# Kernel tuning notes

Measured on AMD Instinct MI355X. Metric: run time of the kernel, lower is better.

Reference implementation:

```python
import jax, jax.numpy as jnp
import numpy as np

N, E, CIN, COUT, T = 50000, 800000, 64, 64, 12


def setup_inputs() -> dict:
    key = jax.random.key(0)
    k1, k2, k3, k4, k5, k6 = jax.random.split(key, 6)
    x = jax.random.normal(k1, (N, CIN, T), dtype=jnp.float32)
    src = jax.random.randint(k2, (E,), 0, N, dtype=jnp.int32)
    dst = jax.random.randint(k3, (E,), 0, N, dtype=jnp.int32)
    edge_index = jnp.stack([src, dst], axis=0)
    edge_attr = jax.random.uniform(k4, (E,), dtype=jnp.float32)
    W = jax.random.normal(k5, (CIN, COUT), dtype=jnp.float32) / np.sqrt(CIN)
    b = jax.random.normal(k6, (COUT,), dtype=jnp.float32) * 0.01
    return {"x": x, "edge_index": edge_index, "edge_attr": edge_attr, "W": W, "b": b}


def reference(x, edge_index, edge_attr, W, b):
    # GCNConv applied independently to each of T temporal slices, then ReLU.
    n = x.shape[0]
    src, dst = edge_index[0], edge_index[1]
    # add self-loops with weight 1.0 (PyG GCNConv default)
    loop = jnp.arange(n, dtype=src.dtype)
    src_f = jnp.concatenate([src, loop])
    dst_f = jnp.concatenate([dst, loop])
    ew = jnp.concatenate([edge_attr, jnp.ones((n,), x.dtype)])
    # symmetric normalization: deg computed at target (col) nodes
    deg = jax.ops.segment_sum(ew, dst_f, num_segments=n)
    dis = jnp.where(deg > 0, jax.lax.rsqrt(deg), 0.0)
    norm = dis[src_f] * ew * dis[dst_f]  # (E+N,)

    def step(carry, x_t):  # x_t: (N, Cin)
        xw = x_t @ W                              # (N, Cout)
        msgs = xw[src_f] * norm[:, None]          # (E+N, Cout) gather
        out = jax.ops.segment_sum(msgs, dst_f, num_segments=n) + b
        return carry, jax.nn.relu(out)

    _, ys = jax.lax.scan(step, None, jnp.transpose(x, (2, 0, 1)))  # (T, N, Cout)
    return jnp.transpose(ys, (1, 2, 0))  # (N, Cout, T)
```

## Files before the change

### kernel.cpp

```cpp
#include <hip/hip_runtime.h>

#define CIN   64
#define COUT  64
#define TT    12
#define FEAT  (CIN * TT)
#define QROW  (FEAT / 4)

typedef unsigned int uint32;
typedef unsigned long long u64;

#define DEG_SCALE 1048576.0f

__global__ __launch_bounds__(256) void k_cvt(const float4* __restrict__ x,
                                             uint2* __restrict__ xh, int nquads) {
    int i = blockIdx.x * blockDim.x + threadIdx.x;
    int stride = gridDim.x * blockDim.x;
    for (; i < nquads; i += stride) {
        float4 v = x[i];
        uint32 u0 = __float_as_uint(v.x), u1 = __float_as_uint(v.y);
        uint32 u2 = __float_as_uint(v.z), u3 = __float_as_uint(v.w);
        u0 = (u0 + 0x7fffu + ((u0 >> 16) & 1)) >> 16;
        u1 = (u1 + 0x7fffu + ((u1 >> 16) & 1)) >> 16;
        u2 = (u2 + 0x7fffu + ((u2 >> 16) & 1)) >> 16;
        u3 = (u3 + 0x7fffu + ((u3 >> 16) & 1)) >> 16;
        uint2 o; o.x = u0 | (u1 << 16); o.y = u2 | (u3 << 16);
        xh[i] = o;
    }
}

__global__ void k_deg(const int* __restrict__ dst, const float* __restrict__ ea,
                      u64* __restrict__ deg64, int e_cnt) {
    int e = blockIdx.x * blockDim.x + threadIdx.x;
    if (e < e_cnt) {
        u64 v = ((u64)1 << 32) | (u64)(uint32)(ea[e] * DEG_SCALE + 0.5f);
        atomicAdd(&deg64[dst[e]], v);
    }
}

__global__ __launch_bounds__(256) void k_disred(const u64* __restrict__ deg64,
                                                float* __restrict__ dis,
                                                int* __restrict__ partial, int n) {
    __shared__ int red[256];
    int t = threadIdx.x;
    int i = blockIdx.x * 256 + t;
    int cnt = 0;
    if (i < n) {
        u64 v = deg64[i];
        cnt = (int)(v >> 32);
        float deg = 1.0f + (float)(uint32)v * (1.0f / DEG_SCALE);
        dis[i] = rsqrtf(deg);
    }
    red[t] = cnt;
    __syncthreads();
    for (int off = 128; off > 0; off >>= 1) {
        if (t < off) red[t] += red[t + off];
        __syncthreads();
    }
    if (t == 0) partial[blockIdx.x] = red[0];
}

__global__ __launch_bounds__(1024) void k_scanpart(int* __restrict__ partial, int nb,
                                                   int* __restrict__ rowptrN) {
    __shared__ int tmp[1024];
    int t = threadIdx.x;
    int v = (t < nb) ? partial[t] : 0;
    tmp[t] = v;
    __syncthreads();
    for (int off = 1; off < 1024; off <<= 1) {
        int u = (t >= off) ? tmp[t - off] : 0;
        __syncthreads();
        tmp[t] += u;
        __syncthreads();
    }
    if (t < nb) partial[t] = tmp[t] - v;
    if (t == 1023) *rowptrN = tmp[1023];
}

__global__ __launch_bounds__(256) void k_scanwrite(const u64* __restrict__ deg64,
                                                   const int* __restrict__ partial,
                                                   int* __restrict__ rowptr,
                                                   int* __restrict__ cursor, int n) {
    __shared__ int tmp[256];
    int t = threadIdx.x;
    int i = blockIdx.x * 256 + t;
    int v = (i < n) ? (int)(deg64[i] >> 32) : 0;
    tmp[t] = v;
    __syncthreads();
    for (int off = 1; off < 256; off <<= 1) {
        int u = (t >= off) ? tmp[t - off] : 0;
        __syncthreads();
        tmp[t] += u;
        __syncthreads();
    }
    int excl = tmp[t] - v + partial[blockIdx.x];
    if (i < n) { rowptr[i] = excl; cursor[i] = excl; }
}

__global__ void k_fill(const int* __restrict__ src, const int* __restrict__ dst,
                       const float* __restrict__ ea, const float* __restrict__ dis,
                       int* __restrict__ cursor, int2* __restrict__ csr, int e_cnt) {
    int e = blockIdx.x * blockDim.x + threadIdx.x;
    if (e < e_cnt) {
        int s = src[e], d = dst[e];
        int pos = atomicAdd(&cursor[d], 1);
        float w = dis[s] * ea[e] * dis[d];
        int2 p; p.x = s; p.y = __float_as_int(w);
        csr[pos] = p;
    }
}

template <int BF16>
__global__ __launch_bounds__(192) void k_conv(
    const void* __restrict__ xsrc, const float* __restrict__ W,
    const float* __restrict__ b, const float* __restrict__ dis,
    const int* __restrict__ rowptr, const int2* __restrict__ csr,
    float* __restrict__ out)
{
    __shared__ float sAgg[FEAT];
    __shared__ float sB[COUT];

    const int n = blockIdx.x;
    const int t = threadIdx.x;
    if (t < COUT) sB[t] = b[t];

    const int start = rowptr[n];
    const int end   = rowptr[n + 1];
    const float dn  = dis[n];
    const float selfw = dn * dn;

    float a0, a1, a2, a3;
    if (BF16) {
        const uint2* xb = (const uint2*)xsrc;
        uint2 v = xb[(size_t)n * QROW + t];
        a0 = selfw * __uint_as_float(v.x << 16);
        a1 = selfw * __uint_as_float(v.x & 0xffff0000u);
        a2 = selfw * __uint_as_float(v.y << 16);
        a3 = selfw * __uint_as_float(v.y & 0xffff0000u);
    } else {
        const float4* xb = (const float4*)xsrc;
        float4 v = xb[(size_t)n * QROW + t];
        a0 = selfw * v.x; a1 = selfw * v.y; a2 = selfw * v.z; a3 = selfw * v.w;
    }

    for (int e = start; e < end; ++e) {
        int2 p = csr[e];
        int s   = p.x;
        float w = __int_as_float(p.y);
        if (BF16) {
            const uint2* xb = (const uint2*)xsrc;
            uint2 v = xb[(size_t)s * QROW + t];
            a0 = fmaf(w, __uint_as_float(v.x << 16),         a0);
            a1 = fmaf(w, __uint_as_float(v.x & 0xffff0000u), a1);
            a2 = fmaf(w, __uint_as_float(v.y << 16),         a2);
            a3 = fmaf(w, __uint_as_float(v.y & 0xffff0000u), a3);
        } else {
            const float4* xb = (const float4*)xsrc;
            float4 v = xb[(size_t)s * QROW + t];
            a0 = fmaf(w, v.x, a0); a1 = fmaf(w, v.y, a1);
            a2 = fmaf(w, v.z, a2); a3 = fmaf(w, v.w, a3);
        }
    }

    float4 av; av.x = a0; av.y = a1; av.z = a2; av.w = a3;
    *((float4*)&sAgg[4 * t]) = av;
    __syncthreads();

    const int co  = t & 63;
    const int tg  = t >> 6;
    const int tt0 = tg * 4;
    float o0 = sB[co], o1 = o0, o2 = o0, o3 = o0;
#pragma unroll
    for (int c = 0; c < CIN; ++c) {
        float wv = W[c * COUT + co];
        o0 = fmaf(wv, sAgg[c * TT + tt0    ], o0);
        o1 = fmaf(wv, sAgg[c * TT + tt0 + 1], o1);
        o2 = fmaf(wv, sAgg[c * TT + tt0 + 2], o2);
        o3 = fmaf(wv, sAgg[c * TT + tt0 + 3], o3);
    }
    o0 = fmaxf(o0, 0.0f); o1 = fmaxf(o1, 0.0f);
    o2 = fmaxf(o2, 0.0f); o3 = fmaxf(o3, 0.0f);

    __syncthreads();
    float4 ov; ov.x = o0; ov.y = o1; ov.z = o2; ov.w = o3;
    *((float4*)&sAgg[co * TT + tt0]) = ov;
    __syncthreads();
    *((float4*)(out + (size_t)n * FEAT + 4 * t)) = *((const float4*)&sAgg[4 * t]);
}

extern "C" void kernel_launch(void* const* d_in, const int* in_sizes, int n_in,
                              void* d_out, int out_size, void* d_ws, size_t ws_size,
                              hipStream_t stream) {
    const float* x   = (const float*)d_in[0];
    const int*   ei  = (const int*)d_in[1];
    const float* ea  = (const float*)d_in[2];
    const float* W   = (const float*)d_in[3];
    const float* b   = (const float*)d_in[4];
    float* out = (float*)d_out;

    const int E = in_sizes[2];
    const int N = in_sizes[0] / FEAT;
    const int* src = ei;
    const int* dst = ei + E;

    size_t off = 0;
    char* ws = (char*)d_ws;
    auto alloc = [&](size_t bytes) -> char* {
        char* p = ws + off;
        off = (off + bytes + 15) & ~(size_t)15;
        return p;
    };
    u64*   deg64   = (u64*)  alloc((size_t)N * 8);
    float* dis     = (float*)alloc((size_t)N * 4);
    int*   rowptr  = (int*)  alloc((size_t)(N + 1) * 4);
    int*   cursor  = (int*)  alloc((size_t)N * 4);
    int*   partial = (int*)  alloc(4096);
    int2*  csr     = (int2*) alloc((size_t)E * 8);
    unsigned short* xh = (unsigned short*)alloc((size_t)N * FEAT * 2);
    const bool use_bf16 = (off <= ws_size);

    int nb_e = (E + 255) / 256;
    int nb_n = (N + 255) / 256;

    hipMemsetAsync(deg64, 0, (size_t)N * 8, stream);
    if (use_bf16) {
        int nquads = (N * FEAT) / 4;
        k_cvt<<<2048, 256, 0, stream>>>((const float4*)x, (uint2*)xh, nquads);
    }
    k_deg      <<<nb_e, 256, 0, stream>>>(dst, ea, deg64, E);
    k_disred   <<<nb_n, 256, 0, stream>>>(deg64, dis, partial, N);
    k_scanpart <<<1, 1024, 0, stream>>>(partial, nb_n, rowptr + N);
    k_scanwrite<<<nb_n, 256, 0, stream>>>(deg64, partial, rowptr, cursor, N);
    k_fill     <<<nb_e, 256, 0, stream>>>(src, dst, ea, dis, cursor, csr, E);
    if (use_bf16)
        k_conv<1><<<N, 192, 0, stream>>>(xh, W, b, dis, rowptr, csr, out);
    else
        k_conv<0><<<N, 192, 0, stream>>>(x,  W, b, dis, rowptr, csr, out);
}
```

Measured before the change: 355.1 us.

## Fuse convert with degree count, merge scan kernels, stage edges in LDS

Merges the bf16 conversion and degree atomics into one launch with block-range dispatch, and folds the single-block partial scan into the per-block scan by having each block reduce its predecessors' partials. The conv kernel now stages CSR entries cooperatively in shared memory in chunks of 192, and uses nontemporal loads and stores for the streaming input and output. The aim is fewer launches and less per-thread redundant CSR loading. The cost is extra barriers in the edge loop, and a scan that assumes at most 256 partial blocks.

```diff
diff --git a/kernel.cpp b/kernel.cpp
--- a/kernel.cpp
+++ b/kernel.cpp
@@ -8,32 +8,36 @@
 
 typedef unsigned int uint32;
 typedef unsigned long long u64;
+typedef float  __attribute__((ext_vector_type(4))) f32x4;
 
 #define DEG_SCALE 1048576.0f
 
-__global__ __launch_bounds__(256) void k_cvt(const float4* __restrict__ x,
-                                             uint2* __restrict__ xh, int nquads) {
-    int i = blockIdx.x * blockDim.x + threadIdx.x;
-    int stride = gridDim.x * blockDim.x;
-    for (; i < nquads; i += stride) {
-        float4 v = x[i];
-        uint32 u0 = __float_as_uint(v.x), u1 = __float_as_uint(v.y);
-        uint32 u2 = __float_as_uint(v.z), u3 = __float_as_uint(v.w);
-        u0 = (u0 + 0x7fffu + ((u0 >> 16) & 1)) >> 16;
-        u1 = (u1 + 0x7fffu + ((u1 >> 16) & 1)) >> 16;
-        u2 = (u2 + 0x7fffu + ((u2 >> 16) & 1)) >> 16;
-        u3 = (u3 + 0x7fffu + ((u3 >> 16) & 1)) >> 16;
-        uint2 o; o.x = u0 | (u1 << 16); o.y = u2 | (u3 << 16);
-        xh[i] = o;
-    }
-}
-
-__global__ void k_deg(const int* __restrict__ dst, const float* __restrict__ ea,
-                      u64* __restrict__ deg64, int e_cnt) {
-    int e = blockIdx.x * blockDim.x + threadIdx.x;
-    if (e < e_cnt) {
-        u64 v = ((u64)1 << 32) | (u64)(uint32)(ea[e] * DEG_SCALE + 0.5f);
-        atomicAdd(&deg64[dst[e]], v);
+__global__ __launch_bounds__(256) void k_cvt_deg(
+    const f32x4* __restrict__ x, uint2* __restrict__ xh, int nquads, int nbCvt,
+    const int* __restrict__ dst, const float* __restrict__ ea,
+    u64* __restrict__ deg64, int e_cnt)
+{
+    int bid = blockIdx.x;
+    if (bid < nbCvt) {
+        int i = bid * 256 + threadIdx.x;
+        int stride = nbCvt * 256;
+        for (; i < nquads; i += stride) {
+            f32x4 v = __builtin_nontemporal_load(&x[i]);
+            uint32 u0 = __float_as_uint(v.x), u1 = __float_as_uint(v.y);
+            uint32 u2 = __float_as_uint(v.z), u3 = __float_as_uint(v.w);
+            u0 = (u0 + 0x7fffu + ((u0 >> 16) & 1)) >> 16;
+            u1 = (u1 + 0x7fffu + ((u1 >> 16) & 1)) >> 16;
+            u2 = (u2 + 0x7fffu + ((u2 >> 16) & 1)) >> 16;
+            u3 = (u3 + 0x7fffu + ((u3 >> 16) & 1)) >> 16;
+            uint2 o; o.x = u0 | (u1 << 16); o.y = u2 | (u3 << 16);
+            xh[i] = o;
+        }
+    } else {
+        int e = (bid - nbCvt) * 256 + threadIdx.x;
+        if (e < e_cnt) {
+            u64 v = ((u64)1 << 32) | (u64)(uint32)(ea[e] * DEG_SCALE + 0.5f);
+            atomicAdd(&deg64[dst[e]], v);
+        }
     }
 }
 
@@ -59,41 +63,36 @@
     if (t == 0) partial[blockIdx.x] = red[0];
 }
 
-__global__ __launch_bounds__(1024) void k_scanpart(int* __restrict__ partial, int nb,
-                                                   int* __restrict__ rowptrN) {
-    __shared__ int tmp[1024];
-    int t = threadIdx.x;
-    int v = (t < nb) ? partial[t] : 0;
-    tmp[t] = v;
-    __syncthreads();
-    for (int off = 1; off < 1024; off <<= 1) {
-        int u = (t >= off) ? tmp[t - off] : 0;
-        __syncthreads();
-        tmp[t] += u;
-        __syncthreads();
-    }
-    if (t < nb) partial[t] = tmp[t] - v;
-    if (t == 1023) *rowptrN = tmp[1023];
-}
-
 __global__ __launch_bounds__(256) void k_scanwrite(const u64* __restrict__ deg64,
                                                    const int* __restrict__ partial,
+                                                   int nb,
                                                    int* __restrict__ rowptr,
                                                    int* __restrict__ cursor, int n) {
     __shared__ int tmp[256];
+    __shared__ int pred[256];
     int t = threadIdx.x;
-    int i = blockIdx.x * 256 + t;
+    int bid = blockIdx.x;
+    int i = bid * 256 + t;
+
+    int pv = (t < nb) ? partial[t] : 0;
+    pred[t] = (t < bid) ? pv : 0;
     int v = (i < n) ? (int)(deg64[i] >> 32) : 0;
     tmp[t] = v;
     __syncthreads();
+    for (int off = 128; off > 0; off >>= 1) {
+        if (t < off) pred[t] += pred[t + off];
+        __syncthreads();
+    }
     for (int off = 1; off < 256; off <<= 1) {
         int u = (t >= off) ? tmp[t - off] : 0;
         __syncthreads();
         tmp[t] += u;
         __syncthreads();
     }
-    int excl = tmp[t] - v + partial[blockIdx.x];
+    int blockOff = pred[0];
+    int excl = tmp[t] - v + blockOff;
     if (i < n) { rowptr[i] = excl; cursor[i] = excl; }
+    if (bid == nb - 1 && t == 255) rowptr[n] = blockOff + tmp[255];
 }
 
 __global__ void k_fill(const int* __restrict__ src, const int* __restrict__ dst,
@@ -117,6 +116,7 @@
     float* __restrict__ out)
 {
     __shared__ float sAgg[FEAT];
+    __shared__ int2  sE[192];
     __shared__ float sB[COUT];
 
     const int n = blockIdx.x;
@@ -137,27 +137,32 @@
         a2 = selfw * __uint_as_float(v.y << 16);
         a3 = selfw * __uint_as_float(v.y & 0xffff0000u);
     } else {
-        const float4* xb = (const float4*)xsrc;
-        float4 v = xb[(size_t)n * QROW + t];
+        const f32x4* xb = (const f32x4*)xsrc;
+        f32x4 v = xb[(size_t)n * QROW + t];
         a0 = selfw * v.x; a1 = selfw * v.y; a2 = selfw * v.z; a3 = selfw * v.w;
     }
 
-    for (int e = start; e < end; ++e) {
-        int2 p = csr[e];
-        int s   = p.x;
-        float w = __int_as_float(p.y);
-        if (BF16) {
-            const uint2* xb = (const uint2*)xsrc;
-            uint2 v = xb[(size_t)s * QROW + t];
-            a0 = fmaf(w, __uint_as_float(v.x << 16),         a0);
-            a1 = fmaf(w, __uint_as_float(v.x & 0xffff0000u), a1);
-            a2 = fmaf(w, __uint_as_float(v.y << 16),         a2);
-            a3 = fmaf(w, __uint_as_float(v.y & 0xffff0000u), a3);
-        } else {
-            const float4* xb = (const float4*)xsrc;
-            float4 v = xb[(size_t)s * QROW + t];
-            a0 = fmaf(w, v.x, a0); a1 = fmaf(w, v.y, a1);
-            a2 = fmaf(w, v.z, a2); a3 = fmaf(w, v.w, a3);
+    for (int base = start; base < end; base += 192) {
+        int cnt = end - base; if (cnt > 192) cnt = 192;
+        __syncthreads();
+        if (t < cnt) sE[t] = csr[base + t];
+        __syncthreads();
+        for (int j = 0; j < cnt; ++j) {
+            int s    = sE[j].x;
+            float w  = __int_as_float(sE[j].y);
+            if (BF16) {
+                const uint2* xb = (const uint2*)xsrc;
+                uint2 v = xb[(size_t)s * QROW + t];
+                a0 = fmaf(w, __uint_as_float(v.x << 16),         a0);
+                a1 = fmaf(w, __uint_as_float(v.x & 0xffff0000u), a1);
+                a2 = fmaf(w, __uint_as_float(v.y << 16),         a2);
+                a3 = fmaf(w, __uint_as_float(v.y & 0xffff0000u), a3);
+            } else {
+                const f32x4* xb = (const f32x4*)xsrc;
+                f32x4 v = xb[(size_t)s * QROW + t];
+                a0 = fmaf(w, v.x, a0); a1 = fmaf(w, v.y, a1);
+                a2 = fmaf(w, v.z, a2); a3 = fmaf(w, v.w, a3);
+            }
         }
     }
 
@@ -184,7 +189,8 @@
     float4 ov; ov.x = o0; ov.y = o1; ov.z = o2; ov.w = o3;
     *((float4*)&sAgg[co * TT + tt0]) = ov;
     __syncthreads();
-    *((float4*)(out + (size_t)n * FEAT + 4 * t)) = *((const float4*)&sAgg[4 * t]);
+    f32x4 r = *((const f32x4*)&sAgg[4 * t]);
+    __builtin_nontemporal_store(r, (f32x4*)(out + (size_t)n * FEAT + 4 * t));
 }
 
 extern "C" void kernel_launch(void* const* d_in, const int* in_sizes, int n_in,
@@ -221,15 +227,17 @@
     int nb_e = (E + 255) / 256;
     int nb_n = (N + 255) / 256;
 
-    hipMemsetAsync(deg64, 0, (size_t)N * 8, stream);
+    (void)hipMemsetAsync(deg64, 0, (size_t)N * 8, stream);
     if (use_bf16) {
         int nquads = (N * FEAT) / 4;
-        k_cvt<<<2048, 256, 0, stream>>>((const float4*)x, (uint2*)xh, nquads);
-    }
-    k_deg      <<<nb_e, 256, 0, stream>>>(dst, ea, deg64, E);
+        int nbCvt = 1024;
+        k_cvt_deg<<<nbCvt + nb_e, 256, 0, stream>>>((const f32x4*)x, (uint2*)xh,
+                                                    nquads, nbCvt, dst, ea, deg64, E);
+    } else {
+        k_cvt_deg<<<nb_e, 256, 0, stream>>>(nullptr, nullptr, 0, 0, dst, ea, deg64, E);
+    }
     k_disred   <<<nb_n, 256, 0, stream>>>(deg64, dis, partial, N);
-    k_scanpart <<<1, 1024, 0, stream>>>(partial, nb_n, rowptr + N);
-    k_scanwrite<<<nb_n, 256, 0, stream>>>(deg64, partial, rowptr, cursor, N);
+    k_scanwrite<<<nb_n, 256, 0, stream>>>(deg64, partial, nb_n, rowptr, cursor, N);
     k_fill     <<<nb_e, 256, 0, stream>>>(src, dst, ea, dis, cursor, csr, E);
     if (use_bf16)
         k_conv<1><<<N, 192, 0, stream>>>(xh, W, b, dis, rowptr, csr, out);
```

Result: faster. 326.7 us (-8.0%).
